# Kernel optimization log

Measured on AMD Instinct MI355X. Metric: run time of the kernel, lower is better.

The kernel has to match this reference:

```python
import math
import jax, jax.numpy as jnp
import numpy as np
from jax import lax

PI = math.pi

def _gauss1d(ks, sigma):
    # kornia gaussian: centered at (ks-1)/2 for both odd and even ks
    x = jnp.arange(ks, dtype=jnp.float32) - (ks - 1) / 2.0
    g = jnp.exp(-0.5 * (x / sigma) ** 2)
    return g / g.sum()

def _unfold_nonoverlap(x, k):
    # F.unfold(x, kernel_size=k, stride=k) for x (B,1,H,W), H,W divisible by k
    B, C, H, W = x.shape
    nH, nW = H // k, W // k
    p = x.reshape(B, nH, k, nW, k).transpose(0, 2, 4, 1, 3)
    return p.reshape(B, k * k, nH * nW)

def _sift(x, ps, nab=8, nsb=4, clipval=0.2, eps=1e-10):
    # kornia SIFTDescriptor(patch_size=ps), x: (N,1,ps,ps) -> (N,128)
    N = x.shape[0]
    g1 = _gauss1d(ps, ps / math.sqrt(2.0))
    gk = jnp.outer(g1, g1)  # (ps,ps), sum 1
    # spatial_gradient mode='diff', normalized, replicate pad
    xp = jnp.pad(x, ((0, 0), (0, 0), (0, 0), (1, 1)), mode='edge')
    gx = 0.5 * (xp[..., 2:] - xp[..., :-2])
    yp = jnp.pad(x, ((0, 0), (0, 0), (1, 1), (0, 0)), mode='edge')
    gy = 0.5 * (yp[:, :, 2:, :] - yp[:, :, :-2, :])
    mag = jnp.sqrt(gx * gx + gy * gy + eps) * gk  # (N,1,ps,ps)
    ori = jnp.arctan2(gy, gx + eps) + 2.0 * PI
    o_big = nab * ori / (2.0 * PI)
    bo0f = jnp.floor(o_big)
    w1 = o_big - bo0f
    bo0 = bo0f.astype(jnp.int32) % nab
    bo1 = (bo0 + 1) % nab
    c0 = jax.nn.one_hot(bo0[:, 0], nab, axis=1, dtype=x.dtype)  # (N,8,ps,ps)
    c1 = jax.nn.one_hot(bo1[:, 0], nab, axis=1, dtype=x.dtype)
    bins = c0 * ((1.0 - w1) * mag) + c1 * (w1 * mag)  # (N,8,ps,ps)
    # triangular pooling kernel, depthwise conv over the 8 angular bins
    bk = 2 * (ps // (nsb + 1)); stride = ps // nsb; pad = bk // 4
    half = bk / 2.0
    xc2 = half - jnp.abs(jnp.arange(bk, dtype=jnp.float32) + 0.5 - half)
    pk = jnp.outer(xc2, xc2) / (half * half)
    pk = jnp.tile(pk[None, None], (nab, 1, 1, 1))  # (8,1,bk,bk)
    pooled = lax.conv_general_dilated(bins, pk, (stride, stride),
        [(pad, pad), (pad, pad)], feature_group_count=nab,
        dimension_numbers=('NCHW', 'OIHW', 'NCHW'))  # (N,8,4,4)
    d = pooled.reshape(N, -1)
    d = d / jnp.maximum(jnp.linalg.norm(d, axis=1, keepdims=True), 1e-12)
    d = jnp.clip(d, 0.0, clipval)
    d = d / jnp.maximum(jnp.linalg.norm(d, axis=1, keepdims=True), 1e-12)
    d = jnp.sqrt(d / jnp.maximum(jnp.abs(d).sum(1, keepdims=True), 1e-12) + eps)  # rootsift
    return d

def _conv_t(x, w, b, stride=2, pad=1):
    # torch ConvTranspose2d; w: (Cin,Cout,k,k)
    k = w.shape[-1]
    wT = jnp.transpose(jnp.flip(w, (-2, -1)), (1, 0, 2, 3))  # (Cout,Cin,k,k)
    y = lax.conv_general_dilated(x, wT, (1, 1),
        [(k - 1 - pad, k - 1 - pad)] * 2, lhs_dilation=(stride, stride),
        dimension_numbers=('NCHW', 'OIHW', 'NCHW'))
    return y + b[None, :, None, None]

def _gn(x, groups, w, b, eps=1e-5):
    N, C, H, W = x.shape
    xg = x.reshape(N, groups, -1)
    mean = xg.mean(-1, keepdims=True)
    var = ((xg - mean) ** 2).mean(-1, keepdims=True)
    xn = ((xg - mean) * lax.rsqrt(var + eps)).reshape(N, C, H, W)
    return xn * w[None, :, None, None] + b[None, :, None, None]

def _jbf(x, guide, ky, kx, sigma_color, sy, sx):
    # kornia joint_bilateral_blur, border='reflect', color_distance='l1'
    B, C, H, W = x.shape
    py, px = ky // 2, kx // 2
    xp = jnp.pad(x, ((0, 0), (0, 0), (py, py), (px, px)), mode='reflect')
    gp = jnp.pad(guide, ((0, 0), (0, 0), (py, py), (px, px)), mode='reflect')
    def win(p):
        return jnp.stack([p[:, :, i:i + H, j:j + W] for i in range(ky) for j in range(kx)], axis=-1)
    ux, ug = win(xp), win(gp)  # (B,C,H,W,ky*kx)
    diff = ug - guide[..., None]
    cd2 = jnp.square(jnp.sum(jnp.abs(diff), axis=1, keepdims=True))
    ck = jnp.exp((-0.5 / (sigma_color ** 2)) * cd2)  # (B,1,H,W,K)
    sk = jnp.outer(_gauss1d(ky, sy), _gauss1d(kx, sx)).reshape(1, 1, 1, 1, -1)
    kern = sk * ck
    return (ux * kern).sum(-1) / kern.sum(-1)

def _forward(x, d1w, d1b, g1w, g1b, s1w, s1b, d2w, d2b, g2w, g2b, s2w, s2b,
             d3w, d3b, g3w, g3b, d4w, d4b, g4w, g4b, fw, fb):
    B = x.shape[0]
    s7 = _sift(_unfold_nonoverlap(x, 7).reshape(-1, 1, 32, 32), 32).reshape(B, 128, 7, 7)
    h = jax.nn.relu(_gn(_conv_t(s7, d1w, d1b), 8, g1w, g1b))  # (B,32,14,14); dropout=identity (eval)
    s14 = _sift(_unfold_nonoverlap(x, 14).reshape(-1, 1, 16, 16), 16).reshape(B, 128, 14, 14)
    sk1 = jnp.einsum('bchw,oc->bohw', s14, s1w[:, :, 0, 0]) + s1b[None, :, None, None]
    h = jax.nn.relu(_gn(_conv_t(jnp.concatenate([h, sk1], 1), d2w, d2b), 4, g2w, g2b))  # (B,16,28,28)
    s28 = _sift(_unfold_nonoverlap(x, 28).reshape(-1, 1, 8, 8), 8).reshape(B, 128, 28, 28)
    sk2 = jnp.einsum('bchw,oc->bohw', s28, s2w[:, :, 0, 0]) + s2b[None, :, None, None]
    h = jax.nn.relu(_gn(_conv_t(jnp.concatenate([h, sk2], 1), d3w, d3b), 2, g3w, g3b))  # (B,8,56,56)
    h = jax.nn.relu(_gn(_conv_t(h, d4w, d4b), 1, g4w, g4b))  # (B,4,112,112)
    h = _conv_t(h, fw, fb)  # (B,2,224,224)
    h = _jbf(h, jnp.tile(x, (1, 2, 1, 1)), 5, 5, 0.1, 1.5, 1.5)
    scale = jnp.array([0.436, 0.615], dtype=h.dtype)
    return jnp.tanh(h) * scale[None, :, None, None]

def setup_inputs() -> dict:
    key = jax.random.key(0)
    ks = jax.random.split(key, 8)
    B = 16
    f32 = jnp.float32
    def rn(k, shp, s=0.05):
        return jax.random.normal(k, shp, f32) * s
    return {
        'x': jax.random.uniform(ks[0], (B, 1, 224, 224), f32),
        'd1w': rn(ks[1], (128, 32, 4, 4)), 'd1b': jnp.zeros((32,), f32),
        'g1w': jnp.ones((32,), f32), 'g1b': jnp.zeros((32,), f32),
        's1w': rn(ks[2], (32, 128, 1, 1)), 's1b': jnp.zeros((32,), f32),
        'd2w': rn(ks[3], (64, 16, 4, 4)), 'd2b': jnp.zeros((16,), f32),
        'g2w': jnp.ones((16,), f32), 'g2b': jnp.zeros((16,), f32),
        's2w': rn(ks[4], (16, 128, 1, 1)), 's2b': jnp.zeros((16,), f32),
        'd3w': rn(ks[5], (32, 8, 4, 4)), 'd3b': jnp.zeros((8,), f32),
        'g3w': jnp.ones((8,), f32), 'g3b': jnp.zeros((8,), f32),
        'd4w': rn(ks[6], (8, 4, 4, 4)), 'd4b': jnp.zeros((4,), f32),
        'g4w': jnp.ones((4,), f32), 'g4b': jnp.zeros((4,), f32),
        'fw': rn(ks[7], (4, 2, 4, 4)), 'fb': jnp.zeros((2,), f32),
    }

def reference(x, d1w, d1b, g1w, g1b, s1w, s1b, d2w, d2b, g2w, g2b, s2w, s2b,
              d3w, d3b, g3w, g3b, d4w, d4b, g4w, g4b, fw, fb):
    return _forward(x, d1w, d1b, g1w, g1b, s1w, s1b, d2w, d2b, g2w, g2b, s2w, s2b,
                    d3w, d3b, g3w, g3b, d4w, d4b, g4w, g4b, fw, fb)
```

## Files before the change

kernel.cpp:

```cpp
#include <hip/hip_runtime.h>
#include <math.h>

#define PI_F 3.14159265358979323846f

template<int PS, int K>
__device__ __forceinline__
void sift_block(const float* __restrict__ x, float* __restrict__ out,
                int n, float* lds)
{
    constexpr int NT = 256;
    constexpr int NPIX = PS*PS;
    constexpr int BK = 2*(PS/5);
    constexpr int STRIDE = PS/4;
    constexpr int PAD = BK/4;
    constexpr float HALF = BK*0.5f;

    float* patch = lds;
    float* c0p   = patch + NPIX;
    float* c1p   = c0p + NPIX;
    float* bo0p  = c1p + NPIX;
    float* pool2 = bo0p + NPIX;

    const int tid = threadIdx.x;
    const int b = n / (K*K);
    const int c = n % (K*K);
    const int ki = c / K;
    const int kj = c % K;

    const float* xb = x + (size_t)b*224*224;
    for (int idx = tid; idx < NPIX; idx += NT) {
        int i = idx / PS, j = idx - i*PS;
        patch[idx] = xb[(i*K + ki)*224 + (j*K + kj)];
    }
    __syncthreads();

    const float inv_sig = 1.0f / ((float)PS * 0.70710678118654752440f);
    for (int idx = tid; idx < NPIX; idx += NT) {
        int i = idx / PS, j = idx - i*PS;
        int jm = j > 0 ? j-1 : 0, jp = j < PS-1 ? j+1 : PS-1;
        int im = i > 0 ? i-1 : 0, ip = i < PS-1 ? i+1 : PS-1;
        float gx = 0.5f*(patch[i*PS+jp] - patch[i*PS+jm]);
        float gy = 0.5f*(patch[ip*PS+j] - patch[im*PS+j]);
        float ti = ((float)i - (PS-1)*0.5f) * inv_sig;
        float tj = ((float)j - (PS-1)*0.5f) * inv_sig;
        float wsp = __expf(-0.5f*(ti*ti + tj*tj));
        float mag = sqrtf(gx*gx + gy*gy + 1e-10f) * wsp;
        float ori = atan2f(gy, gx + 1e-10f) + 2.f*PI_F;
        float ob  = ori * (8.f/(2.f*PI_F));
        float bo0f = floorf(ob);
        float w1 = ob - bo0f;
        int bo0 = ((int)bo0f) & 7;
        c0p[idx]  = (1.f - w1)*mag;
        c1p[idx]  = w1*mag;
        bo0p[idx] = (float)bo0;
    }
    __syncthreads();

    {
        const int win = tid >> 4;
        const int sub = tid & 15;
        const int py = win >> 2;
        const int px = win & 3;
        const int sy = py*STRIDE - PAD;
        const int sx = px*STRIDE - PAD;
        float acc[8];
        #pragma unroll
        for (int o = 0; o < 8; o++) acc[o] = 0.f;

        for (int tap = sub; tap < BK*BK; tap += 16) {
            int di = tap / BK, dj = tap - di*BK;
            int i = sy + di, j = sx + dj;
            if (i < 0 || i >= PS || j < 0 || j >= PS) continue;
            float wgt = (HALF - fabsf((float)di + 0.5f - HALF)) *
                        (HALF - fabsf((float)dj + 0.5f - HALF));
            int idx = i*PS + j;
            float c0 = c0p[idx] * wgt;
            float c1 = c1p[idx] * wgt;
            float bo = bo0p[idx];
            #pragma unroll
            for (int o = 0; o < 8; o++) {
                float ctr = (bo == (float)o) ? c0 :
                            ((bo == (float)((o+7)&7)) ? c1 : 0.f);
                acc[o] += ctr;
            }
        }
        #pragma unroll
        for (int o = 0; o < 8; o++) {
            float v = acc[o];
            v += __shfl_xor(v, 1);
            v += __shfl_xor(v, 2);
            v += __shfl_xor(v, 4);
            v += __shfl_xor(v, 8);
            if (sub == 0) pool2[o*16 + win] = v;
        }
    }
    __syncthreads();

    if (tid < 64) {
        float d0 = pool2[tid];
        float d1 = pool2[tid + 64];

        float s = d0*d0 + d1*d1;
        #pragma unroll
        for (int off = 32; off > 0; off >>= 1) s += __shfl_xor(s, off);
        float nrm = fmaxf(sqrtf(s), 1e-12f);
        d0 /= nrm; d1 /= nrm;
        d0 = fminf(fmaxf(d0, 0.f), 0.2f);
        d1 = fminf(fmaxf(d1, 0.f), 0.2f);
        s = d0*d0 + d1*d1;
        #pragma unroll
        for (int off = 32; off > 0; off >>= 1) s += __shfl_xor(s, off);
        nrm = fmaxf(sqrtf(s), 1e-12f);
        d0 /= nrm; d1 /= nrm;
        s = d0 + d1;
        #pragma unroll
        for (int off = 32; off > 0; off >>= 1) s += __shfl_xor(s, off);
        s = fmaxf(s, 1e-12f);
        d0 = sqrtf(d0/s + 1e-10f);
        d1 = sqrtf(d1/s + 1e-10f);

        out[(size_t)n*128 + tid]      = d0;
        out[(size_t)n*128 + 64 + tid] = d1;
    }
}

__device__ __forceinline__
void sift8_block(const float* __restrict__ x, float* __restrict__ out, int bid)
{
    const int tid = threadIdx.x;
    const int l = tid & 63;
    const int wv = tid >> 6;
    const int n = bid*4 + wv;
    const int b = n / 784;
    const int c = n % 784;
    const int ki = c / 28, kj = c % 28;
    const int i = l >> 3, j = l & 7;

    const float* xb = x + (size_t)b*50176;
    float v = xb[(i*28 + ki)*224 + (j*28 + kj)];

    int lL = (j > 0) ? l-1 : l;
    int lR = (j < 7) ? l+1 : l;
    int lU = (i > 0) ? l-8 : l;
    int lD = (i < 7) ? l+8 : l;
    float pL = __shfl(v, lL);
    float pR = __shfl(v, lR);
    float pU = __shfl(v, lU);
    float pD = __shfl(v, lD);
    float gx = 0.5f*(pR - pL);
    float gy = 0.5f*(pD - pU);

    float ti = ((float)i - 3.5f) * (1.f/5.65685424949238f);
    float tj = ((float)j - 3.5f) * (1.f/5.65685424949238f);
    float wsp = __expf(-0.5f*(ti*ti + tj*tj));
    float mag = sqrtf(gx*gx + gy*gy + 1e-10f) * wsp;
    float ori = atan2f(gy, gx + 1e-10f) + 2.f*PI_F;
    float obig = ori * (8.f/(2.f*PI_F));
    float bo0f = floorf(obig);
    float w1 = obig - bo0f;
    int bo0 = ((int)bo0f) & 7;
    int bo1 = (bo0 + 1) & 7;
    float c0 = (1.f - w1)*mag;
    float c1 = w1*mag;

    const int t = ((i & 1) << 1) | (j & 1);
    float d0 = 0.f, d1 = 0.f;
    #pragma unroll
    for (int o = 0; o < 8; o++) {
        float val = (bo0 == o ? c0 : 0.f) + (bo1 == o ? c1 : 0.f);
        val += __shfl_xor(val, 1);
        val += __shfl_xor(val, 8);
        if (o == 2*t)     d0 = val;
        if (o == 2*t + 1) d1 = val;
    }

    float s = d0*d0 + d1*d1;
    #pragma unroll
    for (int off = 32; off > 0; off >>= 1) s += __shfl_xor(s, off);
    float nrm = fmaxf(sqrtf(s), 1e-12f);
    d0 /= nrm; d1 /= nrm;
    d0 = fminf(fmaxf(d0, 0.f), 0.2f);
    d1 = fminf(fmaxf(d1, 0.f), 0.2f);
    s = d0*d0 + d1*d1;
    #pragma unroll
    for (int off = 32; off > 0; off >>= 1) s += __shfl_xor(s, off);
    nrm = fmaxf(sqrtf(s), 1e-12f);
    d0 /= nrm; d1 /= nrm;
    s = d0 + d1;
    #pragma unroll
    for (int off = 32; off > 0; off >>= 1) s += __shfl_xor(s, off);
    s = fmaxf(s, 1e-12f);
    d0 = sqrtf(d0/s + 1e-10f);
    d1 = sqrtf(d1/s + 1e-10f);

    int cell = (i >> 1)*4 + (j >> 1);
    float* ob = out + (size_t)n*128 + cell;
    ob[(2*t)*16]     = d0;
    ob[(2*t + 1)*16] = d1;
}

__global__ __launch_bounds__(256)
void sift_all(const float* __restrict__ x, float* __restrict__ s7,
              float* __restrict__ s14, float* __restrict__ s28)
{
    __shared__ float lds[4224];
    const int bid = blockIdx.x;
    if (bid < 784) {
        sift_block<32, 7>(x, s7, bid, lds);
    } else if (bid < 3920) {
        sift_block<16, 14>(x, s14, bid - 784, lds);
    } else {
        sift8_block(x, s28, bid - 3920);
    }
}

template<int CO, int S>
__device__ __forceinline__
void conv1x1_block(const float* __restrict__ in, const float* __restrict__ w,
                   const float* __restrict__ bias, float* __restrict__ out,
                   int bid, float* wt)
{
    const int tid = threadIdx.x;
    for (int i = tid; i < 128*CO; i += 256) {
        int c = i / CO, co = i - c*CO;
        wt[i] = w[co*128 + c];
    }
    __syncthreads();
    int idx = bid*256 + tid;
    int s = idx % S; int r = idx / S;
    int co4 = r % (CO/4); int b = r / (CO/4);
    int co = co4*4;
    const float* ib = in + (size_t)b*128*S + s;
    float acc0 = bias[co], acc1 = bias[co+1], acc2 = bias[co+2], acc3 = bias[co+3];
    #pragma unroll 8
    for (int c = 0; c < 128; c++) {
        float v = ib[c*S];
        const float4 wv = *(const float4*)&wt[c*CO + co];
        acc0 += v*wv.x; acc1 += v*wv.y; acc2 += v*wv.z; acc3 += v*wv.w;
    }
    float* ob = out + ((size_t)b*CO + co)*S + s;
    ob[0] = acc0; ob[S] = acc1; ob[2*S] = acc2; ob[3*S] = acc3;
}

__device__ __forceinline__
void convt_l1_block(const float* __restrict__ in0, const float* __restrict__ w,
                    const float* __restrict__ bias,
                    float* __restrict__ out, float2* __restrict__ pst_out,
                    int by, float* lds)
{
    constexpr int CIN = 128, COUT = 32, HIN = 7, NCH = 4, NT = 256;
    constexpr int H0 = 14, SP = 196, HIN2 = 49;
    constexpr int NR = 9, WIN = 9, TILE = CIN*NR*WIN;
    constexpr int WSTRIDE = CIN*NCH*4 + 4;

    float* tile  = lds;
    float* wl2   = tile + TILE;
    float* wpart = wl2 + 4*WSTRIDE;

    const int tid = threadIdx.x;
    const int b  = by >> 3;
    const int cb = by & 7;
    const int c0 = cb*NCH;

    for (int idx = tid; idx < CIN*NCH*16; idx += NT) {
        int tap = idx & 15;
        int t2 = idx >> 4;
        int j = t2 % NCH;
        int ci = t2 / NCH;
        int dy = tap >> 2, dx = tap & 3;
        int pq = (dy & 1)*2 + (dx & 1);
        int k  = (dy >> 1)*2 + (dx >> 1);
        wl2[pq*WSTRIDE + (ci*NCH + j)*4 + k] = w[(ci*COUT + c0 + j)*16 + tap];
    }
    const float* i0 = in0 + (size_t)b*CIN*HIN2;
    for (int idx = tid; idx < TILE; idx += NT) {
        int c = idx % WIN;
        int t2 = idx / WIN;
        int r = t2 % NR;
        int ci = t2 / NR;
        int iy = r - 1, ix = c - 1;
        float v = 0.f;
        if (iy >= 0 && iy < HIN && ix >= 0 && ix < HIN)
            v = i0[ci*HIN2 + iy*HIN + ix];
        tile[idx] = v;
    }
    __syncthreads();

    float acc[NCH];
    #pragma unroll
    for (int j = 0; j < NCH; j++) acc[j] = 0.f;

    const bool active = tid < SP;
    if (active) {
        int oy = tid / H0, ox = tid % H0;
        int pA = (oy+1)&1, qA = (ox+1)&1;
        int iyA = (oy+1-pA)>>1, ixA = (ox+1-qA)>>1;
        int toff = (iyA+1)*WIN + (ixA+1);
        const float* wbase = wl2 + (pA*2+qA)*WSTRIDE;

        #pragma unroll
        for (int j = 0; j < NCH; j++) acc[j] = bias[c0 + j];

        #pragma unroll 4
        for (int ci = 0; ci < CIN; ci++) {
            const float* tp = tile + ci*(NR*WIN) + toff;
            float l0 = tp[0];
            float l1 = tp[-1];
            float l2 = tp[-WIN];
            float l3 = tp[-WIN-1];
            const float* wr = wbase + ci*NCH*4;
            #pragma unroll
            for (int j = 0; j < NCH; j++) {
                const float4 wv = *(const float4*)(wr + j*4);
                acc[j] += l0*wv.x + l1*wv.y + l2*wv.z + l3*wv.w;
            }
        }
        float* ob = out + ((size_t)b*COUT + c0)*SP + tid;
        #pragma unroll
        for (int j = 0; j < NCH; j++) ob[j*SP] = acc[j];
    }

    const int wv = tid >> 6;
    const int ln = tid & 63;
    float ps = 0.f, pq2 = 0.f;
    #pragma unroll
    for (int j = 0; j < NCH; j++) {
        float v = active ? acc[j] : 0.f;
        ps += v; pq2 += v*v;
    }
    #pragma unroll
    for (int off = 32; off > 0; off >>= 1) {
        ps  += __shfl_down(ps,  off);
        pq2 += __shfl_down(pq2, off);
    }
    if (ln == 0) { wpart[wv*2] = ps; wpart[wv*2+1] = pq2; }
    __syncthreads();
    if (tid == 0) {
        float s0 = wpart[0]+wpart[2]+wpart[4]+wpart[6];
        float s1 = wpart[1]+wpart[3]+wpart[5]+wpart[7];
        pst_out[(size_t)b*8 + cb] = make_float2(s0, s1);
    }
}

__global__ __launch_bounds__(256)
void skip_l1(const float* __restrict__ s14, const float* __restrict__ s28,
             const float* __restrict__ s1w, const float* __restrict__ s1b,
             const float* __restrict__ s2w, const float* __restrict__ s2b,
             const float* __restrict__ s7,  const float* __restrict__ d1w,
             const float* __restrict__ d1b,
             float* __restrict__ sk1, float* __restrict__ sk2,
             float* __restrict__ h1, float2* __restrict__ pst1)
{
    __shared__ float lds[18584];
    const int bid = blockIdx.x;
    if (bid < 98)       conv1x1_block<32, 196>(s14, s1w, s1b, sk1, bid, lds);
    else if (bid < 294) conv1x1_block<16, 784>(s28, s2w, s2b, sk2, bid - 98, lds);
    else                convt_l1_block(s7, d1w, d1b, h1, pst1, bid - 294, lds);
}

template<int CIN0, int CIN1, int COUT, int G, int HIN, int NCH, int RT, int NT,
         bool FUSE, int GIN, int NGIN, int NBLK_IN, int NBLK_OUT>
__global__ __launch_bounds__(NT)
void convt_tiled(const float* __restrict__ in0, const float* __restrict__ in1,
                 const float* __restrict__ w, const float* __restrict__ bias,
                 const float2* __restrict__ pst_in,
                 const float* __restrict__ gnw, const float* __restrict__ gnb,
                 float* __restrict__ out, float2* __restrict__ pst_out)
{
    constexpr int CIN = CIN0 + CIN1;
    constexpr int CG = COUT / G;
    constexpr int NGRP = NCH / CG;
    constexpr int CB = COUT / NCH;
    constexpr int H0 = 2*HIN;
    constexpr int SP = H0*H0;
    constexpr int HIN2 = HIN*HIN;
    constexpr int NR = RT/2 + 2;
    constexpr int WIN = HIN + 2;
    constexpr int TILE = CIN*NR*WIN;
    constexpr int WSTRIDE = CIN*NCH*4 + 4;
    constexpr int NPOS = RT*H0;
    constexpr int NWAVE = NT/64;

    __shared__ float tile[TILE];
    __shared__ float wl2[4*WSTRIDE];
    __shared__ float a_s[CIN0];
    __shared__ float b_s[CIN0];
    __shared__ float wpart[NWAVE][NGRP][2];

    const int tid = threadIdx.x;
    const int by = blockIdx.y;
    const int bx = blockIdx.x;
    const int b  = by / CB;
    const int cb = by - b*CB;
    const int c0 = cb*NCH;
    const int g0 = c0 / CG;
    const int r0 = bx * RT;
    const int row0 = r0/2 - 1;

    if constexpr (FUSE) {
        if (tid < CIN0) {
            int gi = tid / (CIN0/GIN);
            float s0 = 0.f, s1 = 0.f;
            for (int k = 0; k < NBLK_IN; k++) {
                float2 p = pst_in[((size_t)b*GIN + gi)*NBLK_IN + k];
                s0 += p.x; s1 += p.y;
            }
            float mean = s0 * (1.f/NGIN);
            float var  = s1 * (1.f/NGIN) - mean*mean;
            float inv  = rsqrtf(var + 1e-5f);
            float a = inv * gnw[tid];
            a_s[tid] = a;
            b_s[tid] = gnb[tid] - mean*a;
        }
        __syncthreads();
    }

    for (int idx = tid; idx < CIN*NCH*16; idx += NT) {
        int tap = idx & 15;
        int t2 = idx >> 4;
        int j = t2 % NCH;
        int ci = t2 / NCH;
        int dy = tap >> 2, dx = tap & 3;
        int pq = (dy & 1)*2 + (dx & 1);
        int k  = (dy >> 1)*2 + (dx >> 1);
        wl2[pq*WSTRIDE + (ci*NCH + j)*4 + k] = w[(ci*COUT + c0 + j)*16 + tap];
    }

    const float* i0 = in0 + (size_t)b*CIN0*HIN2;
    for (int idx = tid; idx < TILE; idx += NT) {
        int c = idx % WIN;
        int t2 = idx / WIN;
        int r = t2 % NR;
        int ci = t2 / NR;
        int iy = row0 + r, ix = c - 1;
        float v = 0.f;
        if (iy >= 0 && iy < HIN && ix >= 0 && ix < HIN) {
            if (CIN1 == 0 || ci < CIN0) {
                v = i0[ci*HIN2 + iy*HIN + ix];
                if constexpr (FUSE) v = fmaxf(v*a_s[ci] + b_s[ci], 0.f);
            } else {
                v = in1[((size_t)b*CIN1 + (ci-CIN0))*HIN2 + iy*HIN + ix];
            }
        }
        tile[idx] = v;
    }
    __syncthreads();

    float acc[NCH];
    #pragma unroll
    for (int j = 0; j < NCH; j++) acc[j] = 0.f;

    const bool active = tid < NPOS;
    if (active) {
        int oy = r0 + tid / H0, ox = tid % H0;
        int pA = (oy+1)&1, qA = (ox+1)&1;
        int iyA = (oy+1-pA)>>1, ixA = (ox+1-qA)>>1;
        int rA = iyA - row0;
        int cA = ixA + 1;
        int toff = rA*WIN + cA;
        const float* wbase = wl2 + (pA*2+qA)*WSTRIDE;

        #pragma unroll
        for (int j = 0; j < NCH; j++) acc[j] = bias[c0 + j];

        #pragma unroll 4
        for (int ci = 0; ci < CIN; ci++) {
            const float* tp = tile + ci*(NR*WIN) + toff;
            float l0 = tp[0];
            float l1 = tp[-1];
            float l2 = tp[-WIN];
            float l3 = tp[-WIN-1];
            const float* wr = wbase + ci*NCH*4;
            #pragma unroll
            for (int j = 0; j < NCH; j++) {
                const float4 wv = *(const float4*)(wr + j*4);
                acc[j] += l0*wv.x + l1*wv.y + l2*wv.z + l3*wv.w;
            }
        }
        float* ob = out + ((size_t)b*COUT + c0)*SP + r0*H0 + tid;
        #pragma unroll
        for (int j = 0; j < NCH; j++) ob[j*SP] = acc[j];
    }

    const int wv = tid >> 6;
    const int ln = tid & 63;
    #pragma unroll
    for (int grp = 0; grp < NGRP; grp++) {
        float ps = 0.f, pq2 = 0.f;
        #pragma unroll
        for (int j = 0; j < CG; j++) {
            float v = active ? acc[grp*CG + j] : 0.f;
            ps += v; pq2 += v*v;
        }
        #pragma unroll
        for (int off = 32; off > 0; off >>= 1) {
            ps  += __shfl_down(ps,  off);
            pq2 += __shfl_down(pq2, off);
        }
        if (ln == 0) { wpart[wv][grp][0] = ps; wpart[wv][grp][1] = pq2; }
    }
    __syncthreads();
    if (tid < NGRP) {
        float s0 = 0.f, s1 = 0.f;
        #pragma unroll
        for (int w2 = 0; w2 < NWAVE; w2++) { s0 += wpart[w2][tid][0]; s1 += wpart[w2][tid][1]; }
        pst_out[((size_t)b*G + g0 + tid)*NBLK_OUT + bx] = make_float2(s0, s1);
    }
}

__global__ __launch_bounds__(256)
void final_bilateral(const float* __restrict__ h4, const float* __restrict__ fw,
                     const float* __restrict__ fb, const float2* __restrict__ pst_in,
                     const float* __restrict__ gnw, const float* __restrict__ gnb,
                     const float* __restrict__ x, float* __restrict__ out)
{
    const float g[5] = {0.1200783f, 0.2338817f, 0.2920800f, 0.2338817f, 0.1200783f};
    __shared__ float xs[400], p0s[400], p1s[400];
    __shared__ float wl2[128];
    __shared__ float a_s[4], b_s[4], bl[2], mv[2];

    const int tid = threadIdx.x;
    const int b = blockIdx.z;
    const int ty0 = blockIdx.y*16;
    const int tx0 = blockIdx.x*16;
    const float* xb = x + (size_t)b*50176;

    if (tid < 128) {
        int k = tid & 3;
        int t = tid >> 2;
        int co = t & 1; t >>= 1;
        int ci = t & 3;
        int pq = t >> 2;
        int pA = pq >> 1, qA = pq & 1;
        int dy = pA + 2*(k>>1), dx = qA + 2*(k&1);
        wl2[tid] = fw[(ci*2 + co)*16 + dy*4 + dx];
    }
    if (tid < 2) bl[tid] = fb[tid];
    if (tid >= 192) {
        int k0 = tid - 192;
        float s0 = 0.f, s1 = 0.f;
        if (k0 < 56) {
            float2 p = pst_in[(size_t)b*56 + k0];
            s0 = p.x; s1 = p.y;
        }
        #pragma unroll
        for (int off = 32; off > 0; off >>= 1) {
            s0 += __shfl_down(s0, off);
            s1 += __shfl_down(s1, off);
        }
        if (k0 == 0) {
            float mean = s0 * (1.f/50176.f);
            float var  = s1 * (1.f/50176.f) - mean*mean;
            mv[0] = mean;
            mv[1] = rsqrtf(var + 1e-5f);
        }
    }
    __syncthreads();
    if (tid < 4) {
        float a = mv[1] * gnw[tid];
        a_s[tid] = a;
        b_s[tid] = gnb[tid] - mv[0]*a;
    }
    __syncthreads();

    const float* ib = h4 + (size_t)b*4*12544;
    for (int idx = tid; idx < 400; idx += 256) {
        int r = idx / 20, cc = idx - r*20;
        int oy = ty0 - 2 + r;  oy = oy < 0 ? -oy : (oy > 223 ? 446 - oy : oy);
        int ox = tx0 - 2 + cc; ox = ox < 0 ? -ox : (ox > 223 ? 446 - ox : ox);
        xs[idx] = xb[oy*224 + ox];

        int pA = (oy+1)&1, iyA = (oy+1-pA)>>1, iyB = iyA-1;
        int qA = (ox+1)&1, ixA = (ox+1-qA)>>1, ixB = ixA-1;
        float mYA = (iyA < 112) ? 1.f : 0.f;
        float mYB = (iyB >= 0)  ? 1.f : 0.f;
        float mXA = (ixA < 112) ? 1.f : 0.f;
        float mXB = (ixB >= 0)  ? 1.f : 0.f;
        float m0 = mYA*mXA, m1 = mYA*mXB, m2 = mYB*mXA, m3 = mYB*mXB;
        int iyAc = min(iyA, 111), iyBc = max(iyB, 0);
        int ixAc = min(ixA, 111), ixBc = max(ixB, 0);
        int oAA = iyAc*112 + ixAc, oAB = iyAc*112 + ixBc;
        int oBA = iyBc*112 + ixAc, oBB = iyBc*112 + ixBc;
        const float* wbase = wl2 + (pA*2+qA)*32;

        float acc0 = bl[0], acc1 = bl[1];
        #pragma unroll
        for (int ci = 0; ci < 4; ci++) {
            const float* ip = ib + ci*12544;
            float a = a_s[ci], bb = b_s[ci];
            float l0 = fmaxf(ip[oAA]*a + bb, 0.f);
            float l1 = fmaxf(ip[oAB]*a + bb, 0.f);
            float l2 = fmaxf(ip[oBA]*a + bb, 0.f);
            float l3 = fmaxf(ip[oBB]*a + bb, 0.f);
            float t0 = l0*m0, t1 = l1*m1, t2 = l2*m2, t3 = l3*m3;
            const float4 w0 = *(const float4*)(wbase + ci*8);
            const float4 w1 = *(const float4*)(wbase + ci*8 + 4);
            acc0 += t0*w0.x + t1*w0.y + t2*w0.z + t3*w0.w;
            acc1 += t0*w1.x + t1*w1.y + t2*w1.z + t3*w1.w;
        }
        p0s[idx] = acc0;
        p1s[idx] = acc1;
    }
    __syncthreads();

    int ly = tid >> 4, lx = tid & 15;
    int base = (ly+2)*20 + (lx+2);
    float center = xs[base];
    float wsum = 0.f, a0 = 0.f, a1 = 0.f;
    #pragma unroll
    for (int di = -2; di <= 2; di++){
        #pragma unroll
        for (int dj = -2; dj <= 2; dj++){
            int o = base + di*20 + dj;
            float dg = xs[o] - center;
            float wgt = g[di+2]*g[dj+2]*__expf(-200.f*dg*dg);
            wsum += wgt;
            a0 += wgt * p0s[o];
            a1 += wgt * p1s[o];
        }
    }
    float inv = 1.0f / wsum;
    int s = (ty0 + ly)*224 + (tx0 + lx);
    out[(size_t)(b*2)*50176 + s]     = tanhf(a0*inv)*0.436f;
    out[(size_t)(b*2+1)*50176 + s]   = tanhf(a1*inv)*0.615f;
}

extern "C" void kernel_launch(void* const* d_in, const int* in_sizes, int n_in,
                              void* d_out, int out_size, void* d_ws, size_t ws_size,
                              hipStream_t stream) {
    (void)in_sizes; (void)n_in; (void)out_size; (void)ws_size;
    const float* x   = (const float*)d_in[0];
    const float* d1w = (const float*)d_in[1];
    const float* d1b = (const float*)d_in[2];
    const float* g1w = (const float*)d_in[3];
    const float* g1b = (const float*)d_in[4];
    const float* s1w = (const float*)d_in[5];
    const float* s1b = (const float*)d_in[6];
    const float* d2w = (const float*)d_in[7];
    const float* d2b = (const float*)d_in[8];
    const float* g2w = (const float*)d_in[9];
    const float* g2b = (const float*)d_in[10];
    const float* s2w = (const float*)d_in[11];
    const float* s2b = (const float*)d_in[12];
    const float* d3w = (const float*)d_in[13];
    const float* d3b = (const float*)d_in[14];
    const float* g3w = (const float*)d_in[15];
    const float* g3b = (const float*)d_in[16];
    const float* d4w = (const float*)d_in[17];
    const float* d4b = (const float*)d_in[18];
    const float* g4w = (const float*)d_in[19];
    const float* g4b = (const float*)d_in[20];
    const float* fw  = (const float*)d_in[21];
    const float* fb  = (const float*)d_in[22];
    float* out = (float*)d_out;

    float* ws  = (float*)d_ws;
    float* s7  = ws;
    float* s14 = s7  + 100352;
    float* s28 = s14 + 401408;
    float* sk1 = s28 + 1605632;
    float* sk2 = sk1 + 100352;
    float* h1  = sk2 + 200704;
    float* h2  = h1  + 100352;
    float* h3  = h2  + 200704;
    float* h4  = h3  + 401408;
    float2* pst1 = (float2*)(h4 + 802816);
    float2* pst2 = pst1 + 128;
    float2* pst3 = pst2 + 448;
    float2* pst4 = pst3 + 448;

    sift_all<<<7056, 256, 0, stream>>>(x, s7, s14, s28);

    skip_l1<<<422, 256, 0, stream>>>(s14, s28, s1w, s1b, s2w, s2b,
                                     s7, d1w, d1b, sk1, sk2, h1, pst1);

    convt_tiled< 32,32, 16, 4, 14, 8,  4, 256, true, 8, 784, 1, 7>
        <<<dim3(7, 16*2), 256, 0, stream>>>(h1, sk1, d2w, d2b, pst1, g1w, g1b, h2, pst2);
    convt_tiled< 16,16,  8, 2, 28, 8,  4, 256, true, 4, 3136, 7, 14>
        <<<dim3(14, 16), 256, 0, stream>>>(h2, sk2, d3w, d3b, pst2, g2w, g2b, h3, pst3);
    convt_tiled<  8, 0,  4, 1, 56, 4,  2, 256, true, 2, 12544, 14, 56>
        <<<dim3(56, 16), 256, 0, stream>>>(h3, nullptr, d4w, d4b, pst3, g3w, g3b, h4, pst4);

    final_bilateral<<<dim3(14, 14, 16), 256, 0, stream>>>(h4, fw, fb, pst4, g4w, g4b, x, out);
}
```

Baseline: 217.5 us.

## Fuse decoder layers and head into one cooperative persistent kernel

Replaces the three transposed-conv launches and the bilateral head launch with a single cooperative kernel of 256 blocks. The blocks loop over virtual block indices and separate the stages with grid-wide syncs, so per-launch overhead and tail gaps between the small kernels go away. Layer 2 also drops from 8 to 4 channels per block, doubling its block count. Shared memory moves to one buffer sized for the largest stage, and a non-cooperative multi-launch path is kept as a fallback. The trade-off is grid.sync cost and only 256 resident blocks doing all the work.

Result: slower. 369.0 us (+69.7%).

```diff
diff --git a/kernel.cpp b/kernel.cpp
--- a/kernel.cpp
+++ b/kernel.cpp
@@ -1,5 +1,8 @@
 #include <hip/hip_runtime.h>
+#include <hip/hip_cooperative_groups.h>
 #include <math.h>
+
+namespace cg = cooperative_groups;
 
 #define PI_F 3.14159265358979323846f
 
@@ -360,12 +363,13 @@
 
 template<int CIN0, int CIN1, int COUT, int G, int HIN, int NCH, int RT, int NT,
          bool FUSE, int GIN, int NGIN, int NBLK_IN, int NBLK_OUT>
-__global__ __launch_bounds__(NT)
-void convt_tiled(const float* __restrict__ in0, const float* __restrict__ in1,
-                 const float* __restrict__ w, const float* __restrict__ bias,
-                 const float2* __restrict__ pst_in,
-                 const float* __restrict__ gnw, const float* __restrict__ gnb,
-                 float* __restrict__ out, float2* __restrict__ pst_out)
+__device__ __forceinline__
+void convt_body(const float* __restrict__ in0, const float* __restrict__ in1,
+                const float* __restrict__ w, const float* __restrict__ bias,
+                const float2* __restrict__ pst_in,
+                const float* __restrict__ gnw, const float* __restrict__ gnb,
+                float* __restrict__ out, float2* __restrict__ pst_out,
+                int by, int bx, float* lds)
 {
     constexpr int CIN = CIN0 + CIN1;
     constexpr int CG = COUT / G;
@@ -381,15 +385,13 @@
     constexpr int NPOS = RT*H0;
     constexpr int NWAVE = NT/64;
 
-    __shared__ float tile[TILE];
-    __shared__ float wl2[4*WSTRIDE];
-    __shared__ float a_s[CIN0];
-    __shared__ float b_s[CIN0];
-    __shared__ float wpart[NWAVE][NGRP][2];
+    float* tile  = lds;
+    float* wl2   = tile + TILE;
+    float* a_s   = wl2 + 4*WSTRIDE;
+    float* b_s   = a_s + CIN0;
+    float* wpart = b_s + CIN0;
 
     const int tid = threadIdx.x;
-    const int by = blockIdx.y;
-    const int bx = blockIdx.x;
     const int b  = by / CB;
     const int cb = by - b*CB;
     const int c0 = cb*NCH;
@@ -497,32 +499,43 @@
             ps  += __shfl_down(ps,  off);
             pq2 += __shfl_down(pq2, off);
         }
-        if (ln == 0) { wpart[wv][grp][0] = ps; wpart[wv][grp][1] = pq2; }
+        if (ln == 0) { wpart[(wv*NGRP + grp)*2] = ps; wpart[(wv*NGRP + grp)*2 + 1] = pq2; }
     }
     __syncthreads();
     if (tid < NGRP) {
         float s0 = 0.f, s1 = 0.f;
         #pragma unroll
-        for (int w2 = 0; w2 < NWAVE; w2++) { s0 += wpart[w2][tid][0]; s1 += wpart[w2][tid][1]; }
+        for (int w2 = 0; w2 < NWAVE; w2++) {
+            s0 += wpart[(w2*NGRP + tid)*2];
+            s1 += wpart[(w2*NGRP + tid)*2 + 1];
+        }
         pst_out[((size_t)b*G + g0 + tid)*NBLK_OUT + bx] = make_float2(s0, s1);
     }
-}
-
-__global__ __launch_bounds__(256)
-void final_bilateral(const float* __restrict__ h4, const float* __restrict__ fw,
-                     const float* __restrict__ fb, const float2* __restrict__ pst_in,
-                     const float* __restrict__ gnw, const float* __restrict__ gnb,
-                     const float* __restrict__ x, float* __restrict__ out)
+    __syncthreads();
+}
+
+__device__ __forceinline__
+void head_body(const float* __restrict__ h4, const float* __restrict__ fw,
+               const float* __restrict__ fb, const float2* __restrict__ pst_in,
+               const float* __restrict__ gnw, const float* __restrict__ gnb,
+               const float* __restrict__ x, float* __restrict__ out,
+               int vb, float* lds)
 {
     const float g[5] = {0.1200783f, 0.2338817f, 0.2920800f, 0.2338817f, 0.1200783f};
-    __shared__ float xs[400], p0s[400], p1s[400];
-    __shared__ float wl2[128];
-    __shared__ float a_s[4], b_s[4], bl[2], mv[2];
+    float* xs  = lds;
+    float* p0s = lds + 400;
+    float* p1s = lds + 800;
+    float* wl2 = lds + 1200;
+    float* a_s = lds + 1328;
+    float* b_s = lds + 1332;
+    float* bl  = lds + 1336;
+    float* mv  = lds + 1338;
 
     const int tid = threadIdx.x;
-    const int b = blockIdx.z;
-    const int ty0 = blockIdx.y*16;
-    const int tx0 = blockIdx.x*16;
+    const int b = vb / 196;
+    const int rem = vb - b*196;
+    const int ty0 = (rem / 14)*16;
+    const int tx0 = (rem % 14)*16;
     const float* xb = x + (size_t)b*50176;
 
     if (tid < 128) {
@@ -623,6 +636,91 @@
     int s = (ty0 + ly)*224 + (tx0 + lx);
     out[(size_t)(b*2)*50176 + s]     = tanhf(a0*inv)*0.436f;
     out[(size_t)(b*2+1)*50176 + s]   = tanhf(a1*inv)*0.615f;
+    __syncthreads();
+}
+
+__global__ __launch_bounds__(256)
+void decoder_all(const float* __restrict__ h1,  const float* __restrict__ sk1,
+                 const float* __restrict__ sk2,
+                 const float* __restrict__ d2w, const float* __restrict__ d2b,
+                 const float* __restrict__ g1w, const float* __restrict__ g1b,
+                 const float* __restrict__ d3w, const float* __restrict__ d3b,
+                 const float* __restrict__ g2w, const float* __restrict__ g2b,
+                 const float* __restrict__ d4w, const float* __restrict__ d4b,
+                 const float* __restrict__ g3w, const float* __restrict__ g3b,
+                 const float* __restrict__ fw,  const float* __restrict__ fb,
+                 const float* __restrict__ g4w, const float* __restrict__ g4b,
+                 const float* __restrict__ x,
+                 float* __restrict__ h2, float* __restrict__ h3,
+                 float* __restrict__ h4,
+                 float2* __restrict__ pst1, float2* __restrict__ pst2,
+                 float2* __restrict__ pst3, float2* __restrict__ pst4,
+                 float* __restrict__ out)
+{
+    __shared__ float lds[8448];
+    cg::grid_group grid = cg::this_grid();
+
+    for (int vb = blockIdx.x; vb < 448; vb += gridDim.x)
+        convt_body< 32,32, 16, 4, 14, 4, 4, 256, true, 8, 784, 1, 7>
+            (h1, sk1, d2w, d2b, pst1, g1w, g1b, h2, pst2, vb / 7, vb % 7, lds);
+    grid.sync();
+
+    for (int vb = blockIdx.x; vb < 224; vb += gridDim.x)
+        convt_body< 16,16,  8, 2, 28, 8, 4, 256, true, 4, 3136, 7, 14>
+            (h2, sk2, d3w, d3b, pst2, g2w, g2b, h3, pst3, vb / 14, vb % 14, lds);
+    grid.sync();
+
+    for (int vb = blockIdx.x; vb < 896; vb += gridDim.x)
+        convt_body<  8, 0,  4, 1, 56, 4, 2, 256, true, 2, 12544, 14, 56>
+            (h3, nullptr, d4w, d4b, pst3, g3w, g3b, h4, pst4, vb / 56, vb % 56, lds);
+    grid.sync();
+
+    for (int vb = blockIdx.x; vb < 3136; vb += gridDim.x)
+        head_body(h4, fw, fb, pst4, g4w, g4b, x, out, vb, lds);
+}
+
+__global__ __launch_bounds__(256)
+void l2_kernel(const float* __restrict__ h1, const float* __restrict__ sk1,
+               const float* __restrict__ d2w, const float* __restrict__ d2b,
+               const float2* __restrict__ pst1,
+               const float* __restrict__ g1w, const float* __restrict__ g1b,
+               float* __restrict__ h2, float2* __restrict__ pst2)
+{
+    __shared__ float lds[8448];
+    convt_body< 32,32, 16, 4, 14, 4, 4, 256, true, 8, 784, 1, 7>
+        (h1, sk1, d2w, d2b, pst1, g1w, g1b, h2, pst2, blockIdx.x / 7, blockIdx.x % 7, lds);
+}
+__global__ __launch_bounds__(256)
+void l3_kernel(const float* __restrict__ h2, const float* __restrict__ sk2,
+               const float* __restrict__ d3w, const float* __restrict__ d3b,
+               const float2* __restrict__ pst2,
+               const float* __restrict__ g2w, const float* __restrict__ g2b,
+               float* __restrict__ h3, float2* __restrict__ pst3)
+{
+    __shared__ float lds[8448];
+    convt_body< 16,16,  8, 2, 28, 8, 4, 256, true, 4, 3136, 7, 14>
+        (h2, sk2, d3w, d3b, pst2, g2w, g2b, h3, pst3, blockIdx.x / 14, blockIdx.x % 14, lds);
+}
+__global__ __launch_bounds__(256)
+void l4_kernel(const float* __restrict__ h3,
+               const float* __restrict__ d4w, const float* __restrict__ d4b,
+               const float2* __restrict__ pst3,
+               const float* __restrict__ g3w, const float* __restrict__ g3b,
+               float* __restrict__ h4, float2* __restrict__ pst4)
+{
+    __shared__ float lds[8448];
+    convt_body<  8, 0,  4, 1, 56, 4, 2, 256, true, 2, 12544, 14, 56>
+        (h3, nullptr, d4w, d4b, pst3, g3w, g3b, h4, pst4, blockIdx.x / 56, blockIdx.x % 56, lds);
+}
+__global__ __launch_bounds__(256)
+void head_kernel(const float* __restrict__ h4,
+                 const float* __restrict__ fw, const float* __restrict__ fb,
+                 const float2* __restrict__ pst4,
+                 const float* __restrict__ g4w, const float* __restrict__ g4b,
+                 const float* __restrict__ x, float* __restrict__ out)
+{
+    __shared__ float lds[1344];
+    head_body(h4, fw, fb, pst4, g4w, g4b, x, out, blockIdx.x, lds);
 }
 
 extern "C" void kernel_launch(void* const* d_in, const int* in_sizes, int n_in,
@@ -674,12 +772,25 @@
     skip_l1<<<422, 256, 0, stream>>>(s14, s28, s1w, s1b, s2w, s2b,
                                      s7, d1w, d1b, sk1, sk2, h1, pst1);
 
-    convt_tiled< 32,32, 16, 4, 14, 8,  4, 256, true, 8, 784, 1, 7>
-        <<<dim3(7, 16*2), 256, 0, stream>>>(h1, sk1, d2w, d2b, pst1, g1w, g1b, h2, pst2);
-    convt_tiled< 16,16,  8, 2, 28, 8,  4, 256, true, 4, 3136, 7, 14>
-        <<<dim3(14, 16), 256, 0, stream>>>(h2, sk2, d3w, d3b, pst2, g2w, g2b, h3, pst3);
-    convt_tiled<  8, 0,  4, 1, 56, 4,  2, 256, true, 2, 12544, 14, 56>
-        <<<dim3(56, 16), 256, 0, stream>>>(h3, nullptr, d4w, d4b, pst3, g3w, g3b, h4, pst4);
-
-    final_bilateral<<<dim3(14, 14, 16), 256, 0, stream>>>(h4, fw, fb, pst4, g4w, g4b, x, out);
-}
+    void* args[] = {
+        (void*)&h1, (void*)&sk1, (void*)&sk2,
+        (void*)&d2w, (void*)&d2b, (void*)&g1w, (void*)&g1b,
+        (void*)&d3w, (void*)&d3b, (void*)&g2w, (void*)&g2b,
+        (void*)&d4w, (void*)&d4b, (void*)&g3w, (void*)&g3b,
+        (void*)&fw,  (void*)&fb,  (void*)&g4w, (void*)&g4b,
+        (void*)&x,
+        (void*)&h2, (void*)&h3, (void*)&h4,
+        (void*)&pst1, (void*)&pst2, (void*)&pst3, (void*)&pst4,
+        (void*)&out
+    };
+    hipError_t err = hipLaunchCooperativeKernel((const void*)decoder_all,
+                                                dim3(256), dim3(256),
+                                                args, 0, stream);
+    if (err != hipSuccess) {
+        (void)hipGetLastError();
+        l2_kernel<<<448,  256, 0, stream>>>(h1, sk1, d2w, d2b, pst1, g1w, g1b, h2, pst2);
+        l3_kernel<<<224,  256, 0, stream>>>(h2, sk2, d3w, d3b, pst2, g2w, g2b, h3, pst3);
+        l4_kernel<<<896,  256, 0, stream>>>(h3, d4w, d4b, pst3, g3w, g3b, h4, pst4);
+        head_kernel<<<3136, 256, 0, stream>>>(h4, fw, fb, pst4, g4w, g4b, x, out);
+    }
+}
```
